# Performance work log

Measured on AMD Instinct MI355X. Metric: run time of the kernel, lower is better.

The kernel has to match this reference:

```python
import jax, jax.numpy as jnp
import numpy as np

GROUPS = 32
EPS = 1e-5


def group_norm(x, gamma, beta):
    b, h, w, c = x.shape
    xg = x.reshape(b, h, w, GROUPS, c // GROUPS)
    mean = jnp.mean(xg, axis=(1, 2, 4), keepdims=True)
    var = jnp.var(xg, axis=(1, 2, 4), keepdims=True)
    xn = ((xg - mean) * jax.lax.rsqrt(var + EPS)).reshape(b, h, w, c)
    return xn * gamma + beta


def conv1x1(x, w, b):
    # 1x1 conv == per-pixel dense: [b,h,w,c] x [c,d] -> [b,h,w,d]
    return jnp.einsum('bhwc,cd->bhwd', x, w) + b


def setup_inputs() -> dict:
    key = jax.random.key(0)
    ks = jax.random.split(key, 6)
    B, H, W, C = 4, 64, 64, 512
    s = 1.0 / np.sqrt(C)
    return {
        'x': jax.random.normal(ks[0], (B, H, W, C), jnp.float32),
        'gn_gamma': jnp.ones((C,), jnp.float32),
        'gn_beta': jnp.zeros((C,), jnp.float32),
        'wq': jax.random.normal(ks[1], (C, C), jnp.float32) * s,
        'bq': jnp.zeros((C,), jnp.float32),
        'wk': jax.random.normal(ks[2], (C, C), jnp.float32) * s,
        'bk': jnp.zeros((C,), jnp.float32),
        'wv': jax.random.normal(ks[3], (C, C), jnp.float32) * s,
        'bv': jnp.zeros((C,), jnp.float32),
        'wp': jax.random.normal(ks[4], (C, C), jnp.float32) * s,
        'bp': jnp.zeros((C,), jnp.float32),
    }


def reference(x, gn_gamma, gn_beta, wq, bq, wk, bk, wv, bv, wp, bp):
    b, h, w, c = x.shape
    n = h * w
    h_ = group_norm(x, gn_gamma, gn_beta)
    q = conv1x1(h_, wq, bq).reshape(b, n, c)
    k = conv1x1(h_, wk, bk).reshape(b, n, c)
    v = conv1x1(h_, wv, bv).reshape(b, n, c)
    scale = c ** (-0.5)
    scores = jnp.einsum('bic,bjc->bij', q, k) * scale  # [b, n, n]
    attn = jax.nn.softmax(scores, axis=-1)
    out = jnp.einsum('bij,bjc->bic', attn, v).reshape(b, h, w, c)
    return x + conv1x1(out, wp, bp)
```

## Files before the change

### kernel.cpp

```cpp
#include <hip/hip_runtime.h>
#include <cstdint>


typedef __bf16 bf16_t;
typedef bf16_t bf16x8 __attribute__((ext_vector_type(8)));
typedef float floatx4 __attribute__((ext_vector_type(4)));
typedef int v8i __attribute__((ext_vector_type(8)));

__device__ __forceinline__ uint16_t f2b(float f) {
    uint32_t u = __builtin_bit_cast(uint32_t, f);
    u += 0x7fffu + ((u >> 16) & 1u);
    return (uint16_t)(u >> 16);
}
__device__ __forceinline__ float b2f(uint16_t h) {
    uint32_t u = ((uint32_t)h) << 16;
    return __builtin_bit_cast(float, u);
}
__device__ __forceinline__ unsigned pk_fp8x4(float a, float b, float c, float d) {
    int w = __builtin_amdgcn_cvt_pk_fp8_f32(a, b, 0, false);
    w = __builtin_amdgcn_cvt_pk_fp8_f32(c, d, w, true);
    return (unsigned)w;
}

__device__ __forceinline__ void lds_copy16(void* lds, const void* glob) {
    __builtin_amdgcn_global_load_lds(
        (__attribute__((address_space(1))) void*)(void*)glob,
        (__attribute__((address_space(3))) void*)lds,
        16, 0, 0);
}

__global__ __launch_bounds__(256) void gn_stats(const float* __restrict__ x,
                                                float* __restrict__ stats,
                                                float* __restrict__ lrow) {
    const int bg = blockIdx.x;
    const int tid = threadIdx.x;
    if (tid < 128) lrow[bg * 128 + tid] = 0.f;
    const int b = bg >> 5, g = bg & 31;
    const float* base = x + (long)b * (4096L * 512) + g * 16;
    float s = 0.f, sq = 0.f;
    #pragma unroll 8
    for (int i = 0; i < 64; i++) {
        int idx4 = tid + i * 256;
        int pixel = idx4 >> 2, c4 = idx4 & 3;
        const float4 v = *(const float4*)(base + (long)pixel * 512 + c4 * 4);
        s += v.x + v.y + v.z + v.w;
        sq += v.x * v.x + v.y * v.y + v.z * v.z + v.w * v.w;
    }
    #pragma unroll
    for (int off = 32; off > 0; off >>= 1) {
        s += __shfl_down(s, off);
        sq += __shfl_down(sq, off);
    }
    __shared__ float rs[4], rq[4];
    const int lane = tid & 63, w = tid >> 6;
    if (lane == 0) { rs[w] = s; rq[w] = sq; }
    __syncthreads();
    if (tid == 0) {
        float S = rs[0] + rs[1] + rs[2] + rs[3];
        float Q = rq[0] + rq[1] + rq[2] + rq[3];
        float mean = S * (1.f / 65536.f);
        float var = Q * (1.f / 65536.f) - mean * mean;
        stats[bg * 2 + 0] = mean;
        stats[bg * 2 + 1] = rsqrtf(var + 1e-5f);
    }
}

__global__ __launch_bounds__(256) void gn_apply(const float* __restrict__ x,
                                                const float* __restrict__ stats,
                                                const float* __restrict__ gamma,
                                                const float* __restrict__ beta,
                                                uint16_t* __restrict__ h) {
    const long idx4 = (long)blockIdx.x * 256 + threadIdx.x;
    const long e0 = idx4 * 4;
    const int c = (int)(e0 & 511);
    const int b = (int)(e0 >> 21);
    const float2 st = ((const float2*)stats)[b * 32 + (c >> 4)];
    const float4 v = ((const float4*)x)[idx4];
    const float4 gm = ((const float4*)gamma)[c >> 2];
    const float4 bt = ((const float4*)beta)[c >> 2];
    union { ushort4 u; uint16_t s[4]; } o;
    o.s[0] = f2b((v.x - st.x) * st.y * gm.x + bt.x);
    o.s[1] = f2b((v.y - st.x) * st.y * gm.y + bt.y);
    o.s[2] = f2b((v.z - st.x) * st.y * gm.z + bt.z);
    o.s[3] = f2b((v.w - st.x) * st.y * gm.w + bt.w);
    ((ushort4*)h)[idx4] = o.u;
}

__global__ __launch_bounds__(256) void wcast_transpose(const float* __restrict__ w0,
                                                       const float* __restrict__ w1,
                                                       const float* __restrict__ w2,
                                                       const float* __restrict__ w3,
                                                       uint16_t* __restrict__ out) {
    const float* ws[4] = {w0, w1, w2, w3};
    const float* w = ws[blockIdx.z];
    uint16_t* o = out + (long)blockIdx.z * 512 * 512;
    __shared__ uint16_t t[64][65];
    const int nb = blockIdx.x * 64, kb = blockIdx.y * 64;
    const int lc = threadIdx.x & 63, lg = threadIdx.x >> 6;
    #pragma unroll
    for (int i = 0; i < 16; i++) {
        int r = lg * 16 + i;
        t[lc][r] = f2b(w[(long)(kb + r) * 512 + nb + lc]);
    }
    __syncthreads();
    #pragma unroll
    for (int i = 0; i < 16; i++) {
        int r = lg * 16 + i;
        o[(long)(nb + r) * 512 + kb + lc] = t[r][lc];
    }
}

__global__ __launch_bounds__(256) void qkv_gemm(const uint16_t* __restrict__ h,
                                                const uint16_t* __restrict__ wT,
                                                const float* __restrict__ bq,
                                                const float* __restrict__ bk,
                                                const float* __restrict__ bv,
                                                uint8_t* __restrict__ q,
                                                uint8_t* __restrict__ k,
                                                uint8_t* __restrict__ vt) {
    __shared__ __align__(16) uint16_t smem[128 * 136];
    uint16_t* sA = smem;
    uint16_t* sB = smem + 8192;

    const int tid = threadIdx.x;
    const long m0 = (long)blockIdx.y * 128;
    const int n0 = blockIdx.x * 128;

    const int lane = tid & 63;
    const int wave = tid >> 6;
    const int wm = (wave & 1) * 64;
    const int wn = (wave >> 1) * 64;
    const int fr = lane & 15;
    const int fh = lane >> 4;
    const int sw = fr & 7;

    floatx4 acc[4][4];
    #pragma unroll
    for (int i = 0; i < 4; i++)
        #pragma unroll
        for (int j = 0; j < 4; j++) acc[i][j] = (floatx4){0.f, 0.f, 0.f, 0.f};

    for (int kt = 0; kt < 512; kt += 64) {
        __syncthreads();
        #pragma unroll
        for (int i = 0; i < 4; i++) {
            const int c = i * 256 + tid;
            const int row = c >> 3;
            const int gj = (c & 7) ^ (row & 7);
            lds_copy16(&sA[c * 8], h + (m0 + row) * 512L + kt + gj * 8);
            lds_copy16(&sB[c * 8], wT + (n0 + row) * 512L + kt + gj * 8);
        }
        __syncthreads();
        #pragma unroll
        for (int kk = 0; kk < 64; kk += 32) {
            const int jx = ((fh + (kk >> 3)) ^ sw) * 8;
            bf16x8 av[4], bv_[4];
            #pragma unroll
            for (int mi = 0; mi < 4; mi++)
                av[mi] = *(const bf16x8*)&sA[(wm + mi * 16 + fr) * 64 + jx];
            #pragma unroll
            for (int ni = 0; ni < 4; ni++)
                bv_[ni] = *(const bf16x8*)&sB[(wn + ni * 16 + fr) * 64 + jx];
            #pragma unroll
            for (int mi = 0; mi < 4; mi++)
                #pragma unroll
                for (int ni = 0; ni < 4; ni++)
                    acc[mi][ni] = __builtin_amdgcn_mfma_f32_16x16x32_bf16(
                        av[mi], bv_[ni], acc[mi][ni], 0, 0, 0);
        }
    }

    const int quad = lane >> 4;
    const int w = n0 >> 9;
    const int nc = n0 & 511;
    const float* bias = (w == 0) ? bq : (w == 1) ? bk : bv;
    __syncthreads();
    if (w < 2) {
        #pragma unroll
        for (int ni = 0; ni < 4; ni++) {
            const int col_l = wn + ni * 16 + fr;
            const float bb = bias[nc + col_l];
            #pragma unroll
            for (int mi = 0; mi < 4; mi++) {
                #pragma unroll
                for (int r = 0; r < 4; r++) {
                    const int row_l = wm + mi * 16 + quad * 4 + r;
                    smem[row_l * 136 + col_l] = f2b(acc[mi][ni][r] + bb);
                }
            }
        }
        __syncthreads();
        uint8_t* out = (w == 0) ? q : k;
        #pragma unroll
        for (int it = 0; it < 8; it++) {
            const int row_l = it * 16 + (tid >> 4);
            const int c0 = (tid & 15) * 8;
            const uint4 d = *(const uint4*)&smem[row_l * 136 + c0];
            const uint16_t* e = (const uint16_t*)&d;
            uint2 o;
            o.x = pk_fp8x4(b2f(e[0]), b2f(e[1]), b2f(e[2]), b2f(e[3]));
            o.y = pk_fp8x4(b2f(e[4]), b2f(e[5]), b2f(e[6]), b2f(e[7]));
            *(uint2*)&out[(m0 + row_l) * 512 + nc + c0] = o;
        }
    } else {
        uint8_t* s8 = (uint8_t*)smem;
        #pragma unroll
        for (int ni = 0; ni < 4; ni++) {
            const int ch_l = wn + ni * 16 + fr;
            const float bb = bias[nc + ch_l];
            #pragma unroll
            for (int mi = 0; mi < 4; mi++) {
                const int pix0 = wm + mi * 16 + quad * 4;
                *(unsigned*)&s8[ch_l * 144 + pix0] =
                    pk_fp8x4(acc[mi][ni][0] + bb, acc[mi][ni][1] + bb,
                             acc[mi][ni][2] + bb, acc[mi][ni][3] + bb);
            }
        }
        __syncthreads();
        const long b = m0 >> 12;
        const int pixb = (int)(m0 & 4095);
        uint8_t* vtb = vt + b * (512L * 4096);
        #pragma unroll
        for (int it = 0; it < 4; it++) {
            const int ch_l = it * 32 + (tid >> 3);
            const int p0 = (tid & 7) * 16;
            *(uint4*)&vtb[(long)(nc + ch_l) * 4096 + pixb + p0] =
                *(const uint4*)&s8[ch_l * 144 + p0];
        }
    }
}

template <int MODE>
__global__ __launch_bounds__(256) void gemm_f8(const uint8_t* __restrict__ A,
                                               const uint8_t* __restrict__ B,
                                               void* __restrict__ Cout,
                                               float* __restrict__ lrow,
                                               float scale, int M, int N, int K,
                                               long aStride, long bStride, long cStride) {
    __shared__ __align__(16) uint16_t smem[128 * 136];
    __shared__ float lbuf[128];
    uint8_t* sA = (uint8_t*)smem;
    uint8_t* sB = (uint8_t*)smem + 16384;

    const int tid = threadIdx.x;
    const int bz = blockIdx.z;
    const long m0 = (long)blockIdx.y * 128;
    const long n0 = (long)blockIdx.x * 128;
    const uint8_t* Ab = A + (long)bz * aStride;
    const uint8_t* Bb = B + (long)bz * bStride;

    const int lane = tid & 63;
    const int wave = tid >> 6;
    const int wm = (wave & 1) * 64;
    const int wn = (wave >> 1) * 64;
    const int fr = lane & 15;
    const int quad = lane >> 4;
    const int sw = fr & 7;

    floatx4 acc[4][4];
    #pragma unroll
    for (int i = 0; i < 4; i++)
        #pragma unroll
        for (int j = 0; j < 4; j++) acc[i][j] = (floatx4){0.f, 0.f, 0.f, 0.f};

    const int p0c = (2 * quad) ^ sw;
    const int p1c = (2 * quad + 1) ^ sw;

    for (int kt = 0; kt < K; kt += 128) {
        __syncthreads();
        #pragma unroll
        for (int i = 0; i < 4; i++) {
            const int c = i * 256 + tid;
            const int row = c >> 3;
            const int gj = (c & 7) ^ (row & 7);
            lds_copy16(&sA[c * 16], Ab + (m0 + row) * (long)K + kt + gj * 16);
            lds_copy16(&sB[c * 16], Bb + (n0 + row) * (long)K + kt + gj * 16);
        }
        __syncthreads();
        v8i af[4], bf[4];
        #pragma unroll
        for (int mi = 0; mi < 4; mi++) {
            const int row = wm + mi * 16 + fr;
            const uint4 lo = *(const uint4*)&sA[row * 128 + p0c * 16];
            const uint4 hi = *(const uint4*)&sA[row * 128 + p1c * 16];
            af[mi] = (v8i){(int)lo.x, (int)lo.y, (int)lo.z, (int)lo.w,
                           (int)hi.x, (int)hi.y, (int)hi.z, (int)hi.w};
        }
        #pragma unroll
        for (int ni = 0; ni < 4; ni++) {
            const int row = wn + ni * 16 + fr;
            const uint4 lo = *(const uint4*)&sB[row * 128 + p0c * 16];
            const uint4 hi = *(const uint4*)&sB[row * 128 + p1c * 16];
            bf[ni] = (v8i){(int)lo.x, (int)lo.y, (int)lo.z, (int)lo.w,
                           (int)hi.x, (int)hi.y, (int)hi.z, (int)hi.w};
        }
        #pragma unroll
        for (int mi = 0; mi < 4; mi++)
            #pragma unroll
            for (int ni = 0; ni < 4; ni++)
                acc[mi][ni] = __builtin_amdgcn_mfma_scale_f32_16x16x128_f8f6f4(
                    af[mi], bf[ni], acc[mi][ni], 0, 0,
                    0, 0x7f7f7f7fu, 0, 0x7f7f7f7fu);
    }

    __syncthreads();
    if (MODE == 4) {
        if (tid < 128) lbuf[tid] = lrow[(long)bz * M + m0 + tid];
        __syncthreads();
    }
    #pragma unroll
    for (int ni = 0; ni < 4; ni++) {
        const int col_l = wn + ni * 16 + fr;
        #pragma unroll
        for (int mi = 0; mi < 4; mi++) {
            #pragma unroll
            for (int r = 0; r < 4; r++) {
                const int row_l = wm + mi * 16 + quad * 4 + r;
                float v = acc[mi][ni][r];
                if (MODE == 3) v = exp2f(v * scale);
                if (MODE == 4) v *= __builtin_amdgcn_rcpf(lbuf[row_l]);
                smem[row_l * 136 + col_l] = f2b(v);
            }
        }
    }
    __syncthreads();
    if (MODE == 3) {
        uint8_t* Cb = (uint8_t*)Cout + (long)bz * cStride;
        float* lb = lrow + (long)bz * M;
        #pragma unroll
        for (int it = 0; it < 8; it++) {
            const int row_l = it * 16 + (tid >> 4);
            const int c0 = (tid & 15) * 8;
            const uint4 d = *(const uint4*)&smem[row_l * 136 + c0];
            const uint16_t* e = (const uint16_t*)&d;
            float f[8];
            float ps = 0.f;
            #pragma unroll
            for (int j = 0; j < 8; j++) { f[j] = b2f(e[j]); ps += f[j]; }
            uint2 o;
            o.x = pk_fp8x4(f[0], f[1], f[2], f[3]);
            o.y = pk_fp8x4(f[4], f[5], f[6], f[7]);
            *(uint2*)&Cb[(m0 + row_l) * (long)N + n0 + c0] = o;
            #pragma unroll
            for (int off = 1; off < 16; off <<= 1) ps += __shfl_xor(ps, off);
            if ((tid & 15) == 0) atomicAdd(&lb[m0 + row_l], ps);
        }
    } else {
        uint16_t* Cb = (uint16_t*)Cout + (long)bz * cStride;
        #pragma unroll
        for (int it = 0; it < 8; it++) {
            const int row_l = it * 16 + (tid >> 4);
            const int c0 = (tid & 15) * 8;
            *(uint4*)&Cb[(m0 + row_l) * (long)N + n0 + c0] =
                *(const uint4*)&smem[row_l * 136 + c0];
        }
    }
}

__global__ __launch_bounds__(256) void gemm_proj(const uint16_t* __restrict__ A,
                                                 const uint16_t* __restrict__ B,
                                                 float* __restrict__ Cout,
                                                 const float* __restrict__ bias,
                                                 const float* __restrict__ resid) {
    __shared__ __align__(16) uint16_t smem[128 * 136];
    uint16_t* sA = smem;
    uint16_t* sB = smem + 8192;
    const int N = 512;

    const int tid = threadIdx.x;
    const long m0 = (long)blockIdx.y * 128;
    const long n0 = (long)blockIdx.x * 128;

    const int lane = tid & 63;
    const int wave = tid >> 6;
    const int wm = (wave & 1) * 64;
    const int wn = (wave >> 1) * 64;
    const int fr = lane & 15;
    const int fh = lane >> 4;
    const int sw = fr & 7;

    floatx4 acc[4][4];
    #pragma unroll
    for (int i = 0; i < 4; i++)
        #pragma unroll
        for (int j = 0; j < 4; j++) acc[i][j] = (floatx4){0.f, 0.f, 0.f, 0.f};

    for (int kt = 0; kt < 512; kt += 64) {
        __syncthreads();
        #pragma unroll
        for (int i = 0; i < 4; i++) {
            const int c = i * 256 + tid;
            const int row = c >> 3;
            const int gj = (c & 7) ^ (row & 7);
            lds_copy16(&sA[c * 8], A + (m0 + row) * 512L + kt + gj * 8);
            lds_copy16(&sB[c * 8], B + (n0 + row) * 512L + kt + gj * 8);
        }
        __syncthreads();
        #pragma unroll
        for (int kk = 0; kk < 64; kk += 32) {
            const int jx = ((fh + (kk >> 3)) ^ sw) * 8;
            bf16x8 av[4], bv[4];
            #pragma unroll
            for (int mi = 0; mi < 4; mi++)
                av[mi] = *(const bf16x8*)&sA[(wm + mi * 16 + fr) * 64 + jx];
            #pragma unroll
            for (int ni = 0; ni < 4; ni++)
                bv[ni] = *(const bf16x8*)&sB[(wn + ni * 16 + fr) * 64 + jx];
            #pragma unroll
            for (int mi = 0; mi < 4; mi++)
                #pragma unroll
                for (int ni = 0; ni < 4; ni++)
                    acc[mi][ni] = __builtin_amdgcn_mfma_f32_16x16x32_bf16(
                        av[mi], bv[ni], acc[mi][ni], 0, 0, 0);
        }
    }

    const int quad = lane >> 4;
    #pragma unroll
    for (int ni = 0; ni < 4; ni++) {
        const long col = n0 + wn + ni * 16 + fr;
        const float bv_ = bias[col];
        #pragma unroll
        for (int mi = 0; mi < 4; mi++) {
            #pragma unroll
            for (int r = 0; r < 4; r++) {
                const long row = m0 + wm + mi * 16 + quad * 4 + r;
                Cout[row * N + col] = acc[mi][ni][r] + bv_ + resid[row * N + col];
            }
        }
    }
}

extern "C" void kernel_launch(void* const* d_in, const int* in_sizes, int n_in,
                              void* d_out, int out_size, void* d_ws, size_t ws_size,
                              hipStream_t stream) {
    const float* x  = (const float*)d_in[0];
    const float* gg = (const float*)d_in[1];
    const float* gb = (const float*)d_in[2];
    const float* wq = (const float*)d_in[3];
    const float* bq = (const float*)d_in[4];
    const float* wk = (const float*)d_in[5];
    const float* bk = (const float*)d_in[6];
    const float* wv = (const float*)d_in[7];
    const float* bv = (const float*)d_in[8];
    const float* wp = (const float*)d_in[9];
    const float* bp = (const float*)d_in[10];
    float* out = (float*)d_out;

    char* ws = (char*)d_ws;
    size_t off = 0;
    auto alloc = [&](size_t bytes) {
        char* p = ws + off;
        off += (bytes + 255) & ~(size_t)255;
        return p;
    };
    float*    stats = (float*)alloc(128 * 2 * sizeof(float));
    float*    lrow  = (float*)alloc(16384L * 4);
    uint16_t* h     = (uint16_t*)alloc(16384L * 512 * 2);
    uint16_t* wT    = (uint16_t*)alloc(4L * 512 * 512 * 2);
    uint8_t*  q8    = (uint8_t*)alloc(16384L * 512);
    uint8_t*  k8    = (uint8_t*)alloc(16384L * 512);
    uint8_t*  vt8   = (uint8_t*)alloc(16384L * 512);
    uint8_t*  sc8   = (uint8_t*)alloc(4L * 4096 * 4096);
    uint16_t* ao    = (uint16_t*)alloc(16384L * 512 * 2);
    if (off > ws_size) return;

    gn_stats<<<128, 256, 0, stream>>>(x, stats, lrow);
    gn_apply<<<8192, 256, 0, stream>>>(x, stats, gg, gb, h);
    wcast_transpose<<<dim3(8, 8, 4), 256, 0, stream>>>(wq, wk, wv, wp, wT);

    qkv_gemm<<<dim3(12, 128), 256, 0, stream>>>(h, wT, bq, bk, bv, q8, k8, vt8);
    const float qscale = 0.06375871540654937f;
    gemm_f8<3><<<dim3(32, 32, 4), 256, 0, stream>>>(q8, k8, sc8, lrow, qscale,
                                                    4096, 4096, 512,
                                                    4096L * 512, 4096L * 512, 4096L * 4096);
    gemm_f8<4><<<dim3(4, 32, 4), 256, 0, stream>>>(sc8, vt8, ao, lrow, 1.f,
                                                   4096, 512, 4096,
                                                   4096L * 4096, 512L * 4096, 4096L * 512);
    gemm_proj<<<dim3(4, 128), 256, 0, stream>>>(ao, wT + 3 * 262144, out, bp, x);
}
```

Before: 310.0 us.

## Double fp8 GEMM K-tile to 256 and defer softmax normalization into projection

The fp8 attention GEMMs now stage a 256-deep K slice per iteration in a 64KB LDS buffer with a new XOR swizzle and 32-byte fragment loads. This halves the number of barrier-separated load phases and doubles MFMA work per sync. The softmax 1/l row normalization moves from the PV GEMM epilogue into the output projection epilogue, and the exp values are truncated rather than rounded to bf16. The larger LDS footprint can reduce the number of resident blocks per CU.

```diff
diff --git a/kernel.cpp b/kernel.cpp
--- a/kernel.cpp
+++ b/kernel.cpp
@@ -237,10 +237,10 @@
                                                float* __restrict__ lrow,
                                                float scale, int M, int N, int K,
                                                long aStride, long bStride, long cStride) {
-    __shared__ __align__(16) uint16_t smem[128 * 136];
-    __shared__ float lbuf[128];
-    uint8_t* sA = (uint8_t*)smem;
-    uint8_t* sB = (uint8_t*)smem + 16384;
+    __shared__ __align__(32) uint8_t smem8[65536];
+    uint8_t* sA = smem8;
+    uint8_t* sB = smem8 + 32768;
+    uint16_t* tile = (uint16_t*)smem8;
 
     const int tid = threadIdx.x;
     const int bz = blockIdx.z;
@@ -255,7 +255,6 @@
     const int wn = (wave >> 1) * 64;
     const int fr = lane & 15;
     const int quad = lane >> 4;
-    const int sw = fr & 7;
 
     floatx4 acc[4][4];
     #pragma unroll
@@ -263,51 +262,39 @@
         #pragma unroll
         for (int j = 0; j < 4; j++) acc[i][j] = (floatx4){0.f, 0.f, 0.f, 0.f};
 
-    const int p0c = (2 * quad) ^ sw;
-    const int p1c = (2 * quad + 1) ^ sw;
-
-    for (int kt = 0; kt < K; kt += 128) {
-        __syncthreads();
-        #pragma unroll
-        for (int i = 0; i < 4; i++) {
+    const int pj = (quad ^ ((fr >> 1) & 3)) * 32;
+
+    for (int kt = 0; kt < K; kt += 256) {
+        __syncthreads();
+        #pragma unroll
+        for (int i = 0; i < 8; i++) {
             const int c = i * 256 + tid;
-            const int row = c >> 3;
-            const int gj = (c & 7) ^ (row & 7);
+            const int row = c >> 4;
+            const int gj = (c & 15) ^ (row & 6);
             lds_copy16(&sA[c * 16], Ab + (m0 + row) * (long)K + kt + gj * 16);
             lds_copy16(&sB[c * 16], Bb + (n0 + row) * (long)K + kt + gj * 16);
         }
         __syncthreads();
-        v8i af[4], bf[4];
-        #pragma unroll
-        for (int mi = 0; mi < 4; mi++) {
-            const int row = wm + mi * 16 + fr;
-            const uint4 lo = *(const uint4*)&sA[row * 128 + p0c * 16];
-            const uint4 hi = *(const uint4*)&sA[row * 128 + p1c * 16];
-            af[mi] = (v8i){(int)lo.x, (int)lo.y, (int)lo.z, (int)lo.w,
-                           (int)hi.x, (int)hi.y, (int)hi.z, (int)hi.w};
-        }
-        #pragma unroll
-        for (int ni = 0; ni < 4; ni++) {
-            const int row = wn + ni * 16 + fr;
-            const uint4 lo = *(const uint4*)&sB[row * 128 + p0c * 16];
-            const uint4 hi = *(const uint4*)&sB[row * 128 + p1c * 16];
-            bf[ni] = (v8i){(int)lo.x, (int)lo.y, (int)lo.z, (int)lo.w,
-                           (int)hi.x, (int)hi.y, (int)hi.z, (int)hi.w};
-        }
-        #pragma unroll
-        for (int mi = 0; mi < 4; mi++)
+        #pragma unroll
+        for (int ks = 0; ks < 2; ks++) {
+            v8i af[4], bf[4];
+            #pragma unroll
+            for (int mi = 0; mi < 4; mi++)
+                af[mi] = *(const v8i*)&sA[(wm + mi * 16 + fr) * 256 + ks * 128 + pj];
             #pragma unroll
             for (int ni = 0; ni < 4; ni++)
-                acc[mi][ni] = __builtin_amdgcn_mfma_scale_f32_16x16x128_f8f6f4(
-                    af[mi], bf[ni], acc[mi][ni], 0, 0,
-                    0, 0x7f7f7f7fu, 0, 0x7f7f7f7fu);
+                bf[ni] = *(const v8i*)&sB[(wn + ni * 16 + fr) * 256 + ks * 128 + pj];
+            #pragma unroll
+            for (int mi = 0; mi < 4; mi++)
+                #pragma unroll
+                for (int ni = 0; ni < 4; ni++)
+                    acc[mi][ni] = __builtin_amdgcn_mfma_scale_f32_16x16x128_f8f6f4(
+                        af[mi], bf[ni], acc[mi][ni], 0, 0,
+                        0, 0x7f7f7f7fu, 0, 0x7f7f7f7fu);
+        }
     }
 
     __syncthreads();
-    if (MODE == 4) {
-        if (tid < 128) lbuf[tid] = lrow[(long)bz * M + m0 + tid];
-        __syncthreads();
-    }
     #pragma unroll
     for (int ni = 0; ni < 4; ni++) {
         const int col_l = wn + ni * 16 + fr;
@@ -317,9 +304,13 @@
             for (int r = 0; r < 4; r++) {
                 const int row_l = wm + mi * 16 + quad * 4 + r;
                 float v = acc[mi][ni][r];
-                if (MODE == 3) v = exp2f(v * scale);
-                if (MODE == 4) v *= __builtin_amdgcn_rcpf(lbuf[row_l]);
-                smem[row_l * 136 + col_l] = f2b(v);
+                if (MODE == 3) {
+                    v = exp2f(v * scale);
+                    tile[row_l * 136 + col_l] =
+                        (uint16_t)(__builtin_bit_cast(uint32_t, v) >> 16);
+                } else {
+                    tile[row_l * 136 + col_l] = f2b(v);
+                }
             }
         }
     }
@@ -331,7 +322,7 @@
         for (int it = 0; it < 8; it++) {
             const int row_l = it * 16 + (tid >> 4);
             const int c0 = (tid & 15) * 8;
-            const uint4 d = *(const uint4*)&smem[row_l * 136 + c0];
+            const uint4 d = *(const uint4*)&tile[row_l * 136 + c0];
             const uint16_t* e = (const uint16_t*)&d;
             float f[8];
             float ps = 0.f;
@@ -352,7 +343,7 @@
             const int row_l = it * 16 + (tid >> 4);
             const int c0 = (tid & 15) * 8;
             *(uint4*)&Cb[(m0 + row_l) * (long)N + n0 + c0] =
-                *(const uint4*)&smem[row_l * 136 + c0];
+                *(const uint4*)&tile[row_l * 136 + c0];
         }
     }
 }
@@ -361,8 +352,10 @@
                                                  const uint16_t* __restrict__ B,
                                                  float* __restrict__ Cout,
                                                  const float* __restrict__ bias,
-                                                 const float* __restrict__ resid) {
+                                                 const float* __restrict__ resid,
+                                                 const float* __restrict__ lrow) {
     __shared__ __align__(16) uint16_t smem[128 * 136];
+    __shared__ float lbuf[128];
     uint16_t* sA = smem;
     uint16_t* sB = smem + 8192;
     const int N = 512;
@@ -370,6 +363,8 @@
     const int tid = threadIdx.x;
     const long m0 = (long)blockIdx.y * 128;
     const long n0 = (long)blockIdx.x * 128;
+
+    if (tid < 128) lbuf[tid] = lrow[m0 + tid];
 
     const int lane = tid & 63;
     const int wave = tid >> 6;
@@ -424,8 +419,10 @@
         for (int mi = 0; mi < 4; mi++) {
             #pragma unroll
             for (int r = 0; r < 4; r++) {
-                const long row = m0 + wm + mi * 16 + quad * 4 + r;
-                Cout[row * N + col] = acc[mi][ni][r] + bv_ + resid[row * N + col];
+                const int rl = wm + mi * 16 + quad * 4 + r;
+                const long row = m0 + rl;
+                const float inv = __builtin_amdgcn_rcpf(lbuf[rl]);
+                Cout[row * N + col] = acc[mi][ni][r] * inv + bv_ + resid[row * N + col];
             }
         }
     }
@@ -477,5 +474,5 @@
     gemm_f8<4><<<dim3(4, 32, 4), 256, 0, stream>>>(sc8, vt8, ao, lrow, 1.f,
                                                    4096, 512, 4096,
                                                    4096L * 4096, 512L * 4096, 4096L * 512);
-    gemm_proj<<<dim3(4, 128), 256, 0, stream>>>(ao, wT + 3 * 262144, out, bp, x);
-}
+    gemm_proj<<<dim3(4, 128), 256, 0, stream>>>(ao, wT + 3 * 262144, out, bp, x, lrow);
+}
```

Result: slower. 335.8 us (+8.3%).

## Move QKV projection to FP8 MFMA and merge prep kernels

Applied to the files above, without the earlier changes.

Group-norm output and the Q/K/V weights are now quantized to FP8 (weights pre-scaled by 16), and the QKV projection runs on the FP8 scaled MFMA instead of bf16. Group-norm statistics and the weight cast/transpose are merged into one prep launch, which removes a kernel launch. The softmax row normalization moves from the PV GEMM into the output projection epilogue, and PV uses a different grid. The aim is less memory traffic and higher matrix throughput, at the cost of lower precision in the projections.

```diff
diff --git a/kernel.cpp b/kernel.cpp
--- a/kernel.cpp
+++ b/kernel.cpp
@@ -20,6 +20,9 @@
     int w = __builtin_amdgcn_cvt_pk_fp8_f32(a, b, 0, false);
     w = __builtin_amdgcn_cvt_pk_fp8_f32(c, d, w, true);
     return (unsigned)w;
+}
+__device__ __forceinline__ uint8_t to_fp8(float a) {
+    return (uint8_t)(__builtin_amdgcn_cvt_pk_fp8_f32(a, a, 0, false) & 0xff);
 }
 
 __device__ __forceinline__ void lds_copy16(void* lds, const void* glob) {
@@ -29,39 +32,77 @@
         16, 0, 0);
 }
 
-__global__ __launch_bounds__(256) void gn_stats(const float* __restrict__ x,
-                                                float* __restrict__ stats,
-                                                float* __restrict__ lrow) {
-    const int bg = blockIdx.x;
+__global__ __launch_bounds__(256) void prep(const float* __restrict__ x,
+                                            float* __restrict__ stats,
+                                            float* __restrict__ lrow,
+                                            const float* __restrict__ w0,
+                                            const float* __restrict__ w1,
+                                            const float* __restrict__ w2,
+                                            const float* __restrict__ w3,
+                                            uint8_t* __restrict__ w8,
+                                            uint16_t* __restrict__ wp16) {
+    __shared__ float tf[64][65];
+    __shared__ float rs[4], rq[4];
     const int tid = threadIdx.x;
-    if (tid < 128) lrow[bg * 128 + tid] = 0.f;
-    const int b = bg >> 5, g = bg & 31;
-    const float* base = x + (long)b * (4096L * 512) + g * 16;
-    float s = 0.f, sq = 0.f;
-    #pragma unroll 8
-    for (int i = 0; i < 64; i++) {
-        int idx4 = tid + i * 256;
-        int pixel = idx4 >> 2, c4 = idx4 & 3;
-        const float4 v = *(const float4*)(base + (long)pixel * 512 + c4 * 4);
-        s += v.x + v.y + v.z + v.w;
-        sq += v.x * v.x + v.y * v.y + v.z * v.z + v.w * v.w;
-    }
-    #pragma unroll
-    for (int off = 32; off > 0; off >>= 1) {
-        s += __shfl_down(s, off);
-        sq += __shfl_down(sq, off);
-    }
-    __shared__ float rs[4], rq[4];
-    const int lane = tid & 63, w = tid >> 6;
-    if (lane == 0) { rs[w] = s; rq[w] = sq; }
-    __syncthreads();
-    if (tid == 0) {
-        float S = rs[0] + rs[1] + rs[2] + rs[3];
-        float Q = rq[0] + rq[1] + rq[2] + rq[3];
-        float mean = S * (1.f / 65536.f);
-        float var = Q * (1.f / 65536.f) - mean * mean;
-        stats[bg * 2 + 0] = mean;
-        stats[bg * 2 + 1] = rsqrtf(var + 1e-5f);
+    const int blk = blockIdx.x;
+    if (blk < 128) {
+        const int bg = blk;
+        if (tid < 128) lrow[bg * 128 + tid] = 0.f;
+        const int b = bg >> 5, g = bg & 31;
+        const float* base = x + (long)b * (4096L * 512) + g * 16;
+        float s = 0.f, sq = 0.f;
+        #pragma unroll 8
+        for (int i = 0; i < 64; i++) {
+            int idx4 = tid + i * 256;
+            int pixel = idx4 >> 2, c4 = idx4 & 3;
+            const float4 v = *(const float4*)(base + (long)pixel * 512 + c4 * 4);
+            s += v.x + v.y + v.z + v.w;
+            sq += v.x * v.x + v.y * v.y + v.z * v.z + v.w * v.w;
+        }
+        #pragma unroll
+        for (int off = 32; off > 0; off >>= 1) {
+            s += __shfl_down(s, off);
+            sq += __shfl_down(sq, off);
+        }
+        const int lane = tid & 63, w = tid >> 6;
+        if (lane == 0) { rs[w] = s; rq[w] = sq; }
+        __syncthreads();
+        if (tid == 0) {
+            float S = rs[0] + rs[1] + rs[2] + rs[3];
+            float Q = rq[0] + rq[1] + rq[2] + rq[3];
+            float mean = S * (1.f / 65536.f);
+            float var = Q * (1.f / 65536.f) - mean * mean;
+            stats[bg * 2 + 0] = mean;
+            stats[bg * 2 + 1] = rsqrtf(var + 1e-5f);
+        }
+    } else {
+        const int t = blk - 128;
+        const int z = t >> 6;
+        const int tt = t & 63;
+        const int nb = (tt & 7) * 64, kb = (tt >> 3) * 64;
+        const float* ws[4] = {w0, w1, w2, w3};
+        const float* w = ws[z];
+        const int lc = tid & 63, lg = tid >> 6;
+        #pragma unroll
+        for (int i = 0; i < 16; i++) {
+            int r = lg * 16 + i;
+            tf[lc][r] = w[(long)(kb + r) * 512 + nb + lc];
+        }
+        __syncthreads();
+        if (z < 3) {
+            uint8_t* o = w8 + (long)z * 512 * 512;
+            #pragma unroll
+            for (int i = 0; i < 16; i++) {
+                int r = lg * 16 + i;
+                o[(long)(nb + r) * 512 + kb + lc] = to_fp8(16.f * tf[r][lc]);
+            }
+        } else {
+            #pragma unroll
+            for (int i = 0; i < 16; i++) {
+                int r = lg * 16 + i;
+                wp16[(long)(nb + r) * 512 + kb + lc] = f2b(tf[r][lc]);
+            }
+        }
     }
 }
 
@@ -69,7 +110,7 @@
                                                 const float* __restrict__ stats,
                                                 const float* __restrict__ gamma,
                                                 const float* __restrict__ beta,
-                                                uint16_t* __restrict__ h) {
+                                                uint8_t* __restrict__ h) {
     const long idx4 = (long)blockIdx.x * 256 + threadIdx.x;
     const long e0 = idx4 * 4;
     const int c = (int)(e0 & 511);
@@ -78,53 +119,369 @@
     const float4 v = ((const float4*)x)[idx4];
     const float4 gm = ((const float4*)gamma)[c >> 2];
     const float4 bt = ((const float4*)beta)[c >> 2];
-    union { ushort4 u; uint16_t s[4]; } o;
-    o.s[0] = f2b((v.x - st.x) * st.y * gm.x + bt.x);
-    o.s[1] = f2b((v.y - st.x) * st.y * gm.y + bt.y);
-    o.s[2] = f2b((v.z - st.x) * st.y * gm.z + bt.z);
-    o.s[3] = f2b((v.w - st.x) * st.y * gm.w + bt.w);
-    ((ushort4*)h)[idx4] = o.u;
-}
-
-__global__ __launch_bounds__(256) void wcast_transpose(const float* __restrict__ w0,
-                                                       const float* __restrict__ w1,
-                                                       const float* __restrict__ w2,
-                                                       const float* __restrict__ w3,
-                                                       uint16_t* __restrict__ out) {
-    const float* ws[4] = {w0, w1, w2, w3};
-    const float* w = ws[blockIdx.z];
-    uint16_t* o = out + (long)blockIdx.z * 512 * 512;
-    __shared__ uint16_t t[64][65];
-    const int nb = blockIdx.x * 64, kb = blockIdx.y * 64;
-    const int lc = threadIdx.x & 63, lg = threadIdx.x >> 6;
-    #pragma unroll
-    for (int i = 0; i < 16; i++) {
-        int r = lg * 16 + i;
-        t[lc][r] = f2b(w[(long)(kb + r) * 512 + nb + lc]);
-    }
-    __syncthreads();
-    #pragma unroll
-    for (int i = 0; i < 16; i++) {
-        int r = lg * 16 + i;
-        o[(long)(nb + r) * 512 + kb + lc] = t[r][lc];
-    }
-}
-
-__global__ __launch_bounds__(256) void qkv_gemm(const uint16_t* __restrict__ h,
-                                                const uint16_t* __restrict__ wT,
-                                                const float* __restrict__ bq,
-                                                const float* __restrict__ bk,
-                                                const float* __restrict__ bv,
-                                                uint8_t* __restrict__ q,
-                                                uint8_t* __restrict__ k,
-                                                uint8_t* __restrict__ vt) {
-    __shared__ __align__(16) uint16_t smem[128 * 136];
-    uint16_t* sA = smem;
-    uint16_t* sB = smem + 8192;
+    ((unsigned*)h)[idx4] = pk_fp8x4((v.x - st.x) * st.y * gm.x + bt.x,
+                                    (v.y - st.x) * st.y * gm.y + bt.y,
+                                    (v.z - st.x) * st.y * gm.z + bt.z,
+                                    (v.w - st.x) * st.y * gm.w + bt.w);
+}
+
+__global__ __launch_bounds__(256) void qkv_f8(const uint8_t* __restrict__ h,
+                                              const uint8_t* __restrict__ w8,
+                                              const float* __restrict__ bq,
+                                              const float* __restrict__ bk,
+                                              const float* __restrict__ bv,
+                                              uint8_t* __restrict__ q,
+                                              uint8_t* __restrict__ k,
+                                              uint8_t* __restrict__ vt) {
+    __shared__ __align__(16) uint8_t smem8[34816];
+    uint8_t* sA = smem8;
+    uint8_t* sB = smem8 + 16384;
+    uint16_t* tile = (uint16_t*)smem8;
 
     const int tid = threadIdx.x;
     const long m0 = (long)blockIdx.y * 128;
     const int n0 = blockIdx.x * 128;
+
+    const int lane = tid & 63;
+    const int wave = tid >> 6;
+    const int wm = (wave & 1) * 64;
+    const int wn = (wave >> 1) * 64;
+    const int fr = lane & 15;
+    const int quad = lane >> 4;
+    const int sw = fr & 7;
+
+    floatx4 acc[4][4];
+    #pragma unroll
+    for (int i = 0; i < 4; i++)
+        #pragma unroll
+        for (int j = 0; j < 4; j++) acc[i][j] = (floatx4){0.f, 0.f, 0.f, 0.f};
+
+    const int p0c = (2 * quad) ^ sw;
+    const int p1c = (2 * quad + 1) ^ sw;
+
+    for (int kt = 0; kt < 512; kt += 128) {
+        __syncthreads();
+        #pragma unroll
+        for (int i = 0; i < 4; i++) {
+            const int c = i * 256 + tid;
+            const int row = c >> 3;
+            const int gj = (c & 7) ^ (row & 7);
+            lds_copy16(&sA[c * 16], h + (m0 + row) * 512L + kt + gj * 16);
+            lds_copy16(&sB[c * 16], w8 + (n0 + row) * 512L + kt + gj * 16);
+        }
+        __syncthreads();
+        v8i af[4], bf[4];
+        #pragma unroll
+        for (int mi = 0; mi < 4; mi++) {
+            const int row = wm + mi * 16 + fr;
+            const uint4 lo = *(const uint4*)&sA[row * 128 + p0c * 16];
+            const uint4 hi = *(const uint4*)&sA[row * 128 + p1c * 16];
+            af[mi] = (v8i){(int)lo.x, (int)lo.y, (int)lo.z, (int)lo.w,
+                           (int)hi.x, (int)hi.y, (int)hi.z, (int)hi.w};
+        }
+        #pragma unroll
+        for (int ni = 0; ni < 4; ni++) {
+            const int row = wn + ni * 16 + fr;
+            const uint4 lo = *(const uint4*)&sB[row * 128 + p0c * 16];
+            const uint4 hi = *(const uint4*)&sB[row * 128 + p1c * 16];
+            bf[ni] = (v8i){(int)lo.x, (int)lo.y, (int)lo.z, (int)lo.w,
+                           (int)hi.x, (int)hi.y, (int)hi.z, (int)hi.w};
+        }
+        #pragma unroll
+        for (int mi = 0; mi < 4; mi++)
+            #pragma unroll
+            for (int ni = 0; ni < 4; ni++)
+                acc[mi][ni] = __builtin_amdgcn_mfma_scale_f32_16x16x128_f8f6f4(
+                    af[mi], bf[ni], acc[mi][ni], 0, 0,
+                    0, 0x7f7f7f7fu, 0, 0x7f7f7f7fu);
+    }
+
+    const int w = n0 >> 9;
+    const int nc = n0 & 511;
+    const float* bias = (w == 0) ? bq : (w == 1) ? bk : bv;
+    __syncthreads();
+    if (w < 2) {
+        #pragma unroll
+        for (int ni = 0; ni < 4; ni++) {
+            const int col_l = wn + ni * 16 + fr;
+            const float bb = bias[nc + col_l];
+            #pragma unroll
+            for (int mi = 0; mi < 4; mi++) {
+                #pragma unroll
+                for (int r = 0; r < 4; r++) {
+                    const int row_l = wm + mi * 16 + quad * 4 + r;
+                    tile[row_l * 136 + col_l] = f2b(acc[mi][ni][r] * 0.0625f + bb);
+                }
+            }
+        }
+        __syncthreads();
+        uint8_t* out = (w == 0) ? q : k;
+        #pragma unroll
+        for (int it = 0; it < 8; it++) {
+            const int row_l = it * 16 + (tid >> 4);
+            const int c0 = (tid & 15) * 8;
+            const uint4 d = *(const uint4*)&tile[row_l * 136 + c0];
+            const uint16_t* e = (const uint16_t*)&d;
+            uint2 o;
+            o.x = pk_fp8x4(b2f(e[0]), b2f(e[1]), b2f(e[2]), b2f(e[3]));
+            o.y = pk_fp8x4(b2f(e[4]), b2f(e[5]), b2f(e[6]), b2f(e[7]));
+            *(uint2*)&out[(m0 + row_l) * 512 + nc + c0] = o;
+        }
+    } else {
+        uint8_t* s8 = smem8;
+        #pragma unroll
+        for (int ni = 0; ni < 4; ni++) {
+            const int ch_l = wn + ni * 16 + fr;
+            const float bb = bias[nc + ch_l];
+            #pragma unroll
+            for (int mi = 0; mi < 4; mi++) {
+                const int pix0 = wm + mi * 16 + quad * 4;
+                *(unsigned*)&s8[ch_l * 144 + pix0] =
+                    pk_fp8x4(acc[mi][ni][0] * 0.0625f + bb,
+                             acc[mi][ni][1] * 0.0625f + bb,
+                             acc[mi][ni][2] * 0.0625f + bb,
+                             acc[mi][ni][3] * 0.0625f + bb);
+            }
+        }
+        __syncthreads();
+        const long b = m0 >> 12;
+        const int pixb = (int)(m0 & 4095);
+        uint8_t* vtb = vt + b * (512L * 4096);
+        #pragma unroll
+        for (int it = 0; it < 4; it++) {
+            const int ch_l = it * 32 + (tid >> 3);
+            const int p0 = (tid & 7) * 16;
+            *(uint4*)&vtb[(long)(nc + ch_l) * 4096 + pixb + p0] =
+                *(const uint4*)&s8[ch_l * 144 + p0];
+        }
+    }
+}
+
+__global__ __launch_bounds__(256) void scores_f8(const uint8_t* __restrict__ A,
+                                                 const uint8_t* __restrict__ B,
+                                                 uint8_t* __restrict__ Cout,
+                                                 float* __restrict__ lrow,
+                                                 float scale) {
+    __shared__ __align__(16) uint8_t smem8[34816];
+    uint8_t* sA = smem8;
+    uint8_t* sB = smem8 + 16384;
+    uint16_t* tile = (uint16_t*)smem8;
+
+    const int tid = threadIdx.x;
+    const int bz = blockIdx.z;
+    const long m0 = (long)blockIdx.y * 128;
+    const long n0 = (long)blockIdx.x * 128;
+    const uint8_t* Ab = A + (long)bz * (4096L * 512);
+    const uint8_t* Bb = B + (long)bz * (4096L * 512);
+
+    const int lane = tid & 63;
+    const int wave = tid >> 6;
+    const int wm = (wave & 1) * 64;
+    const int wn = (wave >> 1) * 64;
+    const int fr = lane & 15;
+    const int quad = lane >> 4;
+    const int sw = fr & 7;
+
+    floatx4 acc[4][4];
+    #pragma unroll
+    for (int i = 0; i < 4; i++)
+        #pragma unroll
+        for (int j = 0; j < 4; j++) acc[i][j] = (floatx4){0.f, 0.f, 0.f, 0.f};
+
+    const int p0c = (2 * quad) ^ sw;
+    const int p1c = (2 * quad + 1) ^ sw;
+
+    for (int kt = 0; kt < 512; kt += 128) {
+        __syncthreads();
+        #pragma unroll
+        for (int i = 0; i < 4; i++) {
+            const int c = i * 256 + tid;
+            const int row = c >> 3;
+            const int gj = (c & 7) ^ (row & 7);
+            lds_copy16(&sA[c * 16], Ab + (m0 + row) * 512L + kt + gj * 16);
+            lds_copy16(&sB[c * 16], Bb + (n0 + row) * 512L + kt + gj * 16);
+        }
+        __syncthreads();
+        v8i af[4], bf[4];
+        #pragma unroll
+        for (int mi = 0; mi < 4; mi++) {
+            const int row = wm + mi * 16 + fr;
+            const uint4 lo = *(const uint4*)&sA[row * 128 + p0c * 16];
+            const uint4 hi = *(const uint4*)&sA[row * 128 + p1c * 16];
+            af[mi] = (v8i){(int)lo.x, (int)lo.y, (int)lo.z, (int)lo.w,
+                           (int)hi.x, (int)hi.y, (int)hi.z, (int)hi.w};
+        }
+        #pragma unroll
+        for (int ni = 0; ni < 4; ni++) {
+            const int row = wn + ni * 16 + fr;
+            const uint4 lo = *(const uint4*)&sB[row * 128 + p0c * 16];
+            const uint4 hi = *(const uint4*)&sB[row * 128 + p1c * 16];
+            bf[ni] = (v8i){(int)lo.x, (int)lo.y, (int)lo.z, (int)lo.w,
+                           (int)hi.x, (int)hi.y, (int)hi.z, (int)hi.w};
+        }
+        #pragma unroll
+        for (int mi = 0; mi < 4; mi++)
+            #pragma unroll
+            for (int ni = 0; ni < 4; ni++)
+                acc[mi][ni] = __builtin_amdgcn_mfma_scale_f32_16x16x128_f8f6f4(
+                    af[mi], bf[ni], acc[mi][ni], 0, 0,
+                    0, 0x7f7f7f7fu, 0, 0x7f7f7f7fu);
+    }
+
+    __syncthreads();
+    #pragma unroll
+    for (int ni = 0; ni < 4; ni++) {
+        const int col_l = wn + ni * 16 + fr;
+        #pragma unroll
+        for (int mi = 0; mi < 4; mi++) {
+            #pragma unroll
+            for (int r = 0; r < 4; r++) {
+                const int row_l = wm + mi * 16 + quad * 4 + r;
+                const float v = exp2f(acc[mi][ni][r] * scale);
+                tile[row_l * 136 + col_l] =
+                    (uint16_t)(__builtin_bit_cast(uint32_t, v) >> 16);
+            }
+        }
+    }
+    __syncthreads();
+    uint8_t* Cb = Cout + (long)bz * (4096L * 4096);
+    float* lb = lrow + (long)bz * 4096;
+    #pragma unroll
+    for (int it = 0; it < 8; it++) {
+        const int row_l = it * 16 + (tid >> 4);
+        const int c0 = (tid & 15) * 8;
+        const uint4 d = *(const uint4*)&tile[row_l * 136 + c0];
+        const uint16_t* e = (const uint16_t*)&d;
+        float f[8];
+        float ps = 0.f;
+        #pragma unroll
+        for (int j = 0; j < 8; j++) { f[j] = b2f(e[j]); ps += f[j]; }
+        uint2 o;
+        o.x = pk_fp8x4(f[0], f[1], f[2], f[3]);
+        o.y = pk_fp8x4(f[4], f[5], f[6], f[7]);
+        *(uint2*)&Cb[(m0 + row_l) * 4096 + n0 + c0] = o;
+        #pragma unroll
+        for (int off = 1; off < 16; off <<= 1) ps += __shfl_xor(ps, off);
+        if ((tid & 15) == 0) atomicAdd(&lb[m0 + row_l], ps);
+    }
+}
+
+__global__ __launch_bounds__(256) void pv_f8(const uint8_t* __restrict__ A,
+                                             const uint8_t* __restrict__ B,
+                                             uint16_t* __restrict__ ao) {
+    __shared__ __align__(16) uint8_t smem8[24576];
+    uint8_t* sA = smem8;
+    uint8_t* sB = smem8 + 16384;
+    uint16_t* tile = (uint16_t*)smem8;
+
+    const int tid = threadIdx.x;
+    const int bz = blockIdx.z;
+    const long m0 = (long)blockIdx.y * 128;
+    const int n0 = blockIdx.x * 64;
+    const uint8_t* Ab = A + (long)bz * (4096L * 4096);
+    const uint8_t* Bb = B + (long)bz * (512L * 4096);
+
+    const int lane = tid & 63;
+    const int wave = tid >> 6;
+    const int wm = (wave & 1) * 64;
+    const int wn = (wave >> 1) * 32;
+    const int fr = lane & 15;
+    const int quad = lane >> 4;
+    const int sw = fr & 7;
+
+    floatx4 acc[4][2];
+    #pragma unroll
+    for (int i = 0; i < 4; i++)
+        #pragma unroll
+        for (int j = 0; j < 2; j++) acc[i][j] = (floatx4){0.f, 0.f, 0.f, 0.f};
+
+    const int p0c = (2 * quad) ^ sw;
+    const int p1c = (2 * quad + 1) ^ sw;
+
+    for (int kt = 0; kt < 4096; kt += 128) {
+        __syncthreads();
+        #pragma unroll
+        for (int i = 0; i < 4; i++) {
+            const int c = i * 256 + tid;
+            const int row = c >> 3;
+            const int gj = (c & 7) ^ (row & 7);
+            lds_copy16(&sA[c * 16], Ab + (m0 + row) * 4096L + kt + gj * 16);
+        }
+        #pragma unroll
+        for (int i = 0; i < 2; i++) {
+            const int c = i * 256 + tid;
+            const int row = c >> 3;
+            const int gj = (c & 7) ^ (row & 7);
+            lds_copy16(&sB[c * 16], Bb + (long)(n0 + row) * 4096 + kt + gj * 16);
+        }
+        __syncthreads();
+        v8i af[4], bf[2];
+        #pragma unroll
+        for (int mi = 0; mi < 4; mi++) {
+            const int row = wm + mi * 16 + fr;
+            const uint4 lo = *(const uint4*)&sA[row * 128 + p0c * 16];
+            const uint4 hi = *(const uint4*)&sA[row * 128 + p1c * 16];
+            af[mi] = (v8i){(int)lo.x, (int)lo.y, (int)lo.z, (int)lo.w,
+                           (int)hi.x, (int)hi.y, (int)hi.z, (int)hi.w};
+        }
+        #pragma unroll
+        for (int ni = 0; ni < 2; ni++) {
+            const int row = wn + ni * 16 + fr;
+            const uint4 lo = *(const uint4*)&sB[row * 128 + p0c * 16];
+            const uint4 hi = *(const uint4*)&sB[row * 128 + p1c * 16];
+            bf[ni] = (v8i){(int)lo.x, (int)lo.y, (int)lo.z, (int)lo.w,
+                           (int)hi.x, (int)hi.y, (int)hi.z, (int)hi.w};
+        }
+        #pragma unroll
+        for (int mi = 0; mi < 4; mi++)
+            #pragma unroll
+            for (int ni = 0; ni < 2; ni++)
+                acc[mi][ni] = __builtin_amdgcn_mfma_scale_f32_16x16x128_f8f6f4(
+                    af[mi], bf[ni], acc[mi][ni], 0, 0,
+                    0, 0x7f7f7f7fu, 0, 0x7f7f7f7fu);
+    }
+
+    __syncthreads();
+    #pragma unroll
+    for (int ni = 0; ni < 2; ni++) {
+        const int col_l = wn + ni * 16 + fr;
+        #pragma unroll
+        for (int mi = 0; mi < 4; mi++) {
+            #pragma unroll
+            for (int r = 0; r < 4; r++) {
+                const int row_l = wm + mi * 16 + quad * 4 + r;
+                tile[row_l * 72 + col_l] = f2b(acc[mi][ni][r]);
+            }
+        }
+    }
+    __syncthreads();
+    uint16_t* aob = ao + (long)bz * (4096L * 512);
+    #pragma unroll
+    for (int it = 0; it < 4; it++) {
+        const int row_l = it * 32 + (tid >> 3);
+        const int c0 = (tid & 7) * 8;
+        *(uint4*)&aob[(m0 + row_l) * 512 + n0 + c0] =
+            *(const uint4*)&tile[row_l * 72 + c0];
+    }
+}
+
+__global__ __launch_bounds__(256) void gemm_proj(const uint16_t* __restrict__ A,
+                                                 const uint16_t* __restrict__ B,
+                                                 float* __restrict__ Cout,
+                                                 const float* __restrict__ bias,
+                                                 const float* __restrict__ resid,
+                                                 const float* __restrict__ lrow) {
+    __shared__ __align__(16) uint16_t smem[128 * 136];
+    __shared__ float lbuf[128];
+    uint16_t* sA = smem;
+    uint16_t* sB = smem + 8192;
+    const int N = 512;
+
+    const int tid = threadIdx.x;
+    const long m0 = (long)blockIdx.y * 128;
+    const long n0 = (long)blockIdx.x * 128;
+
+    if (tid < 128) lbuf[tid] = lrow[m0 + tid];
 
     const int lane = tid & 63;
     const int wave = tid >> 6;
@@ -147,251 +504,6 @@
             const int c = i * 256 + tid;
             const int row = c >> 3;
             const int gj = (c & 7) ^ (row & 7);
-            lds_copy16(&sA[c * 8], h + (m0 + row) * 512L + kt + gj * 8);
-            lds_copy16(&sB[c * 8], wT + (n0 + row) * 512L + kt + gj * 8);
-        }
-        __syncthreads();
-        #pragma unroll
-        for (int kk = 0; kk < 64; kk += 32) {
-            const int jx = ((fh + (kk >> 3)) ^ sw) * 8;
-            bf16x8 av[4], bv_[4];
-            #pragma unroll
-            for (int mi = 0; mi < 4; mi++)
-                av[mi] = *(const bf16x8*)&sA[(wm + mi * 16 + fr) * 64 + jx];
-            #pragma unroll
-            for (int ni = 0; ni < 4; ni++)
-                bv_[ni] = *(const bf16x8*)&sB[(wn + ni * 16 + fr) * 64 + jx];
-            #pragma unroll
-            for (int mi = 0; mi < 4; mi++)
-                #pragma unroll
-                for (int ni = 0; ni < 4; ni++)
-                    acc[mi][ni] = __builtin_amdgcn_mfma_f32_16x16x32_bf16(
-                        av[mi], bv_[ni], acc[mi][ni], 0, 0, 0);
-        }
-    }
-
-    const int quad = lane >> 4;
-    const int w = n0 >> 9;
-    const int nc = n0 & 511;
-    const float* bias = (w == 0) ? bq : (w == 1) ? bk : bv;
-    __syncthreads();
-    if (w < 2) {
-        #pragma unroll
-        for (int ni = 0; ni < 4; ni++) {
-            const int col_l = wn + ni * 16 + fr;
-            const float bb = bias[nc + col_l];
-            #pragma unroll
-            for (int mi = 0; mi < 4; mi++) {
-                #pragma unroll
-                for (int r = 0; r < 4; r++) {
-                    const int row_l = wm + mi * 16 + quad * 4 + r;
-                    smem[row_l * 136 + col_l] = f2b(acc[mi][ni][r] + bb);
-                }
-            }
-        }
-        __syncthreads();
-        uint8_t* out = (w == 0) ? q : k;
-        #pragma unroll
-        for (int it = 0; it < 8; it++) {
-            const int row_l = it * 16 + (tid >> 4);
-            const int c0 = (tid & 15) * 8;
-            const uint4 d = *(const uint4*)&smem[row_l * 136 + c0];
-            const uint16_t* e = (const uint16_t*)&d;
-            uint2 o;
-            o.x = pk_fp8x4(b2f(e[0]), b2f(e[1]), b2f(e[2]), b2f(e[3]));
-            o.y = pk_fp8x4(b2f(e[4]), b2f(e[5]), b2f(e[6]), b2f(e[7]));
-            *(uint2*)&out[(m0 + row_l) * 512 + nc + c0] = o;
-        }
-    } else {
-        uint8_t* s8 = (uint8_t*)smem;
-        #pragma unroll
-        for (int ni = 0; ni < 4; ni++) {
-            const int ch_l = wn + ni * 16 + fr;
-            const float bb = bias[nc + ch_l];
-            #pragma unroll
-            for (int mi = 0; mi < 4; mi++) {
-                const int pix0 = wm + mi * 16 + quad * 4;
-                *(unsigned*)&s8[ch_l * 144 + pix0] =
-                    pk_fp8x4(acc[mi][ni][0] + bb, acc[mi][ni][1] + bb,
-                             acc[mi][ni][2] + bb, acc[mi][ni][3] + bb);
-            }
-        }
-        __syncthreads();
-        const long b = m0 >> 12;
-        const int pixb = (int)(m0 & 4095);
-        uint8_t* vtb = vt + b * (512L * 4096);
-        #pragma unroll
-        for (int it = 0; it < 4; it++) {
-            const int ch_l = it * 32 + (tid >> 3);
-            const int p0 = (tid & 7) * 16;
-            *(uint4*)&vtb[(long)(nc + ch_l) * 4096 + pixb + p0] =
-                *(const uint4*)&s8[ch_l * 144 + p0];
-        }
-    }
-}
-
-template <int MODE>
-__global__ __launch_bounds__(256) void gemm_f8(const uint8_t* __restrict__ A,
-                                               const uint8_t* __restrict__ B,
-                                               void* __restrict__ Cout,
-                                               float* __restrict__ lrow,
-                                               float scale, int M, int N, int K,
-                                               long aStride, long bStride, long cStride) {
-    __shared__ __align__(16) uint16_t smem[128 * 136];
-    __shared__ float lbuf[128];
-    uint8_t* sA = (uint8_t*)smem;
-    uint8_t* sB = (uint8_t*)smem + 16384;
-
-    const int tid = threadIdx.x;
-    const int bz = blockIdx.z;
-    const long m0 = (long)blockIdx.y * 128;
-    const long n0 = (long)blockIdx.x * 128;
-    const uint8_t* Ab = A + (long)bz * aStride;
-    const uint8_t* Bb = B + (long)bz * bStride;
-
-    const int lane = tid & 63;
-    const int wave = tid >> 6;
-    const int wm = (wave & 1) * 64;
-    const int wn = (wave >> 1) * 64;
-    const int fr = lane & 15;
-    const int quad = lane >> 4;
-    const int sw = fr & 7;
-
-    floatx4 acc[4][4];
-    #pragma unroll
-    for (int i = 0; i < 4; i++)
-        #pragma unroll
-        for (int j = 0; j < 4; j++) acc[i][j] = (floatx4){0.f, 0.f, 0.f, 0.f};
-
-    const int p0c = (2 * quad) ^ sw;
-    const int p1c = (2 * quad + 1) ^ sw;
-
-    for (int kt = 0; kt < K; kt += 128) {
-        __syncthreads();
-        #pragma unroll
-        for (int i = 0; i < 4; i++) {
-            const int c = i * 256 + tid;
-            const int row = c >> 3;
-            const int gj = (c & 7) ^ (row & 7);
-            lds_copy16(&sA[c * 16], Ab + (m0 + row) * (long)K + kt + gj * 16);
-            lds_copy16(&sB[c * 16], Bb + (n0 + row) * (long)K + kt + gj * 16);
-        }
-        __syncthreads();
-        v8i af[4], bf[4];
-        #pragma unroll
-        for (int mi = 0; mi < 4; mi++) {
-            const int row = wm + mi * 16 + fr;
-            const uint4 lo = *(const uint4*)&sA[row * 128 + p0c * 16];
-            const uint4 hi = *(const uint4*)&sA[row * 128 + p1c * 16];
-            af[mi] = (v8i){(int)lo.x, (int)lo.y, (int)lo.z, (int)lo.w,
-                           (int)hi.x, (int)hi.y, (int)hi.z, (int)hi.w};
-        }
-        #pragma unroll
-        for (int ni = 0; ni < 4; ni++) {
-            const int row = wn + ni * 16 + fr;
-            const uint4 lo = *(const uint4*)&sB[row * 128 + p0c * 16];
-            const uint4 hi = *(const uint4*)&sB[row * 128 + p1c * 16];
-            bf[ni] = (v8i){(int)lo.x, (int)lo.y, (int)lo.z, (int)lo.w,
-                           (int)hi.x, (int)hi.y, (int)hi.z, (int)hi.w};
-        }
-        #pragma unroll
-        for (int mi = 0; mi < 4; mi++)
-            #pragma unroll
-            for (int ni = 0; ni < 4; ni++)
-                acc[mi][ni] = __builtin_amdgcn_mfma_scale_f32_16x16x128_f8f6f4(
-                    af[mi], bf[ni], acc[mi][ni], 0, 0,
-                    0, 0x7f7f7f7fu, 0, 0x7f7f7f7fu);
-    }
-
-    __syncthreads();
-    if (MODE == 4) {
-        if (tid < 128) lbuf[tid] = lrow[(long)bz * M + m0 + tid];
-        __syncthreads();
-    }
-    #pragma unroll
-    for (int ni = 0; ni < 4; ni++) {
-        const int col_l = wn + ni * 16 + fr;
-        #pragma unroll
-        for (int mi = 0; mi < 4; mi++) {
-            #pragma unroll
-            for (int r = 0; r < 4; r++) {
-                const int row_l = wm + mi * 16 + quad * 4 + r;
-                float v = acc[mi][ni][r];
-                if (MODE == 3) v = exp2f(v * scale);
-                if (MODE == 4) v *= __builtin_amdgcn_rcpf(lbuf[row_l]);
-                smem[row_l * 136 + col_l] = f2b(v);
-            }
-        }
-    }
-    __syncthreads();
-    if (MODE == 3) {
-        uint8_t* Cb = (uint8_t*)Cout + (long)bz * cStride;
-        float* lb = lrow + (long)bz * M;
-        #pragma unroll
-        for (int it = 0; it < 8; it++) {
-            const int row_l = it * 16 + (tid >> 4);
-            const int c0 = (tid & 15) * 8;
-            const uint4 d = *(const uint4*)&smem[row_l * 136 + c0];
-            const uint16_t* e = (const uint16_t*)&d;
-            float f[8];
-            float ps = 0.f;
-            #pragma unroll
-            for (int j = 0; j < 8; j++) { f[j] = b2f(e[j]); ps += f[j]; }
-            uint2 o;
-            o.x = pk_fp8x4(f[0], f[1], f[2], f[3]);
-            o.y = pk_fp8x4(f[4], f[5], f[6], f[7]);
-            *(uint2*)&Cb[(m0 + row_l) * (long)N + n0 + c0] = o;
-            #pragma unroll
-            for (int off = 1; off < 16; off <<= 1) ps += __shfl_xor(ps, off);
-            if ((tid & 15) == 0) atomicAdd(&lb[m0 + row_l], ps);
-        }
-    } else {
-        uint16_t* Cb = (uint16_t*)Cout + (long)bz * cStride;
-        #pragma unroll
-        for (int it = 0; it < 8; it++) {
-            const int row_l = it * 16 + (tid >> 4);
-            const int c0 = (tid & 15) * 8;
-            *(uint4*)&Cb[(m0 + row_l) * (long)N + n0 + c0] =
-                *(const uint4*)&smem[row_l * 136 + c0];
-        }
-    }
-}
-
-__global__ __launch_bounds__(256) void gemm_proj(const uint16_t* __restrict__ A,
-                                                 const uint16_t* __restrict__ B,
-                                                 float* __restrict__ Cout,
-                                                 const float* __restrict__ bias,
-                                                 const float* __restrict__ resid) {
-    __shared__ __align__(16) uint16_t smem[128 * 136];
-    uint16_t* sA = smem;
-    uint16_t* sB = smem + 8192;
-    const int N = 512;
-
-    const int tid = threadIdx.x;
-    const long m0 = (long)blockIdx.y * 128;
-    const long n0 = (long)blockIdx.x * 128;
-
-    const int lane = tid & 63;
-    const int wave = tid >> 6;
-    const int wm = (wave & 1) * 64;
-    const int wn = (wave >> 1) * 64;
-    const int fr = lane & 15;
-    const int fh = lane >> 4;
-    const int sw = fr & 7;
-
-    floatx4 acc[4][4];
-    #pragma unroll
-    for (int i = 0; i < 4; i++)
-        #pragma unroll
-        for (int j = 0; j < 4; j++) acc[i][j] = (floatx4){0.f, 0.f, 0.f, 0.f};
-
-    for (int kt = 0; kt < 512; kt += 64) {
-        __syncthreads();
-        #pragma unroll
-        for (int i = 0; i < 4; i++) {
-            const int c = i * 256 + tid;
-            const int row = c >> 3;
-            const int gj = (c & 7) ^ (row & 7);
             lds_copy16(&sA[c * 8], A + (m0 + row) * 512L + kt + gj * 8);
             lds_copy16(&sB[c * 8], B + (n0 + row) * 512L + kt + gj * 8);
         }
@@ -424,8 +536,10 @@
         for (int mi = 0; mi < 4; mi++) {
             #pragma unroll
             for (int r = 0; r < 4; r++) {
-                const long row = m0 + wm + mi * 16 + quad * 4 + r;
-                Cout[row * N + col] = acc[mi][ni][r] + bv_ + resid[row * N + col];
+                const int rl = wm + mi * 16 + quad * 4 + r;
+                const long row = m0 + rl;
+                const float inv = __builtin_amdgcn_rcpf(lbuf[rl]);
+                Cout[row * N + col] = acc[mi][ni][r] * inv + bv_ + resid[row * N + col];
             }
         }
     }
@@ -456,8 +570,9 @@
     };
     float*    stats = (float*)alloc(128 * 2 * sizeof(float));
     float*    lrow  = (float*)alloc(16384L * 4);
-    uint16_t* h     = (uint16_t*)alloc(16384L * 512 * 2);
-    uint16_t* wT    = (uint16_t*)alloc(4L * 512 * 512 * 2);
+    uint8_t*  h8    = (uint8_t*)alloc(16384L * 512);
+    uint8_t*  w8    = (uint8_t*)alloc(3L * 512 * 512);
+    uint16_t* wp16  = (uint16_t*)alloc(512L * 512 * 2);
     uint8_t*  q8    = (uint8_t*)alloc(16384L * 512);
     uint8_t*  k8    = (uint8_t*)alloc(16384L * 512);
     uint8_t*  vt8   = (uint8_t*)alloc(16384L * 512);
@@ -465,17 +580,11 @@
     uint16_t* ao    = (uint16_t*)alloc(16384L * 512 * 2);
     if (off > ws_size) return;
 
-    gn_stats<<<128, 256, 0, stream>>>(x, stats, lrow);
-    gn_apply<<<8192, 256, 0, stream>>>(x, stats, gg, gb, h);
-    wcast_transpose<<<dim3(8, 8, 4), 256, 0, stream>>>(wq, wk, wv, wp, wT);
-
-    qkv_gemm<<<dim3(12, 128), 256, 0, stream>>>(h, wT, bq, bk, bv, q8, k8, vt8);
+    prep<<<384, 256, 0, stream>>>(x, stats, lrow, wq, wk, wv, wp, w8, wp16);
+    gn_apply<<<8192, 256, 0, stream>>>(x, stats, gg, gb, h8);
+    qkv_f8<<<dim3(12, 128), 256, 0, stream>>>(h8, w8, bq, bk, bv, q8, k8, vt8);
     const float qscale = 0.06375871540654937f;
-    gemm_f8<3><<<dim3(32, 32, 4), 256, 0, stream>>>(q8, k8, sc8, lrow, qscale,
-                                                    4096, 4096, 512,
-                                                    4096L * 512, 4096L * 512, 4096L * 4096);
-    gemm_f8<4><<<dim3(4, 32, 4), 256, 0, stream>>>(sc8, vt8, ao, lrow, 1.f,
-                                                   4096, 512, 4096,
-                                                   4096L * 4096, 512L * 4096, 4096L * 512);
-    gemm_proj<<<dim3(4, 128), 256, 0, stream>>>(ao, wT + 3 * 262144, out, bp, x);
-}
+    scores_f8<<<dim3(32, 32, 4), 256, 0, stream>>>(q8, k8, sc8, lrow, qscale);
+    pv_f8<<<dim3(8, 32, 4), 256, 0, stream>>>(sc8, vt8, ao);
+    gemm_proj<<<dim3(4, 128), 256, 0, stream>>>(ao, wp16, out, bp, x, lrow);
+}
```

Result: slower. 349.2 us (+12.7%).
